# Performance work log

Measured on AMD Instinct MI355X. Metric: run time of the kernel, lower is better.

## Reference

```python
import jax, jax.numpy as jnp
import numpy as np


def ternarize_weight(w):
    # abs-mean threshold quantization to {-am, 0, +am}
    abs_mean = jnp.maximum(jnp.abs(w).mean(), 1e-5)
    thr = 0.7 * abs_mean
    q = jnp.where(w > thr, 1.0, jnp.where(w < -thr, -1.0, 0.0))
    # STE: forward value is q*abs_mean, grad flows to w as identity
    return w + jax.lax.stop_gradient(q * abs_mean - w)


def rotate_half(x):
    x1, x2 = jnp.split(x, 2, axis=-1)
    return jnp.concatenate([-x2, x1], axis=-1)


def setup_inputs() -> dict:
    key = jax.random.key(0)
    k1, k2, k3, k4, k5 = jax.random.split(key, 5)
    B, T, C, H = 2, 2048, 1024, 16
    D = C // H
    x = jax.random.normal(k1, (B, T, C), dtype=jnp.float32)
    cos = jax.random.uniform(k2, (1, 1, T, D), dtype=jnp.float32)
    sin = jax.random.uniform(k3, (1, 1, T, D), dtype=jnp.float32)
    w_qkv = jax.random.normal(k4, (3 * C, C), dtype=jnp.float32) / np.sqrt(C)
    w_proj = jax.random.normal(k5, (C, C), dtype=jnp.float32) / np.sqrt(C)
    return {"x": x, "cos": cos, "sin": sin, "w_qkv": w_qkv, "w_proj": w_proj}


def reference(x, cos, sin, w_qkv, w_proj):
    B, T, C = x.shape
    H = 16
    D = C // H
    wq = ternarize_weight(w_qkv)
    wp = ternarize_weight(w_proj)
    qkv = x @ wq.T  # [B,T,3C]
    q, k, v = jnp.split(qkv, 3, axis=-1)
    # [B,T,C] -> [B,H,T,D]
    q = q.reshape(B, T, H, D).transpose(0, 2, 1, 3)
    k = k.reshape(B, T, H, D).transpose(0, 2, 1, 3)
    v = v.reshape(B, T, H, D).transpose(0, 2, 1, 3)
    # RoPE
    q = q * cos + rotate_half(q) * sin
    k = k * cos + rotate_half(k) * sin
    # causal SDPA
    scale = 1.0 / np.sqrt(D)
    scores = jnp.einsum("bhqd,bhkd->bhqk", q, k) * scale
    causal = jnp.tril(jnp.ones((T, T), dtype=bool))
    scores = jnp.where(causal, scores, jnp.finfo(scores.dtype).min)
    attn = jax.nn.softmax(scores, axis=-1)
    y = jnp.einsum("bhqk,bhkd->bhqd", attn, v)  # [B,H,T,D]
    y = y.transpose(0, 2, 1, 3).reshape(B, T, C)
    return y @ wp.T
```

## Files before the change

kernel.cpp:

```cpp
#include <hip/hip_runtime.h>
#include <hip/hip_bf16.h>

#define B_ 2
#define T_ 2048
#define C_ 1024
#define H_ 16
#define D_ 64
#define M_ 4096
#define N3C 3072

using short8  = __attribute__((ext_vector_type(8))) short;
using floatx4 = __attribute__((ext_vector_type(4))) float;
typedef unsigned int u32;

__device__ __forceinline__ unsigned short f2b(float f) {
  __hip_bfloat16 h = __float2bfloat16(f);
  return *reinterpret_cast<unsigned short*>(&h);
}
__device__ __forceinline__ float b2f(unsigned short u) {
  union { unsigned int i; float f; } x; x.i = ((unsigned int)u) << 16; return x.f;
}
__device__ __forceinline__ u32 pk2(float a, float b) {
  float2 t; t.x = a; t.y = b;
  __hip_bfloat162 p = __float22bfloat162_rn(t);
  return *reinterpret_cast<u32*>(&p);
}

#if __has_builtin(__builtin_amdgcn_exp2f)
__device__ __forceinline__ float ex2(float x) { return __builtin_amdgcn_exp2f(x); }
#else
__device__ __forceinline__ float ex2(float x) { return exp2f(x); }
#endif

__device__ __forceinline__ void gll16(const void* g, void* l) {
  __builtin_amdgcn_global_load_lds((const __attribute__((address_space(1))) u32*)g,
                                   (__attribute__((address_space(3))) u32*)l, 16, 0, 0);
}

#define SYNCV(N) do {                                                   \
    asm volatile("s_waitcnt vmcnt(" #N ")" ::: "memory");               \
    __builtin_amdgcn_s_barrier();                                       \
    asm volatile("" ::: "memory");                                      \
  } while (0)


__global__ void abs_sum2(const float* __restrict__ wq, const float* __restrict__ wp,
                         double* __restrict__ sums) {
  __shared__ double red[4];
  const float* w = blockIdx.y ? wp : wq;
  const int n4 = blockIdx.y ? (C_ * C_ / 4) : (3 * C_ * C_ / 4);
  int stride = gridDim.x * blockDim.x;
  double s = 0.0;
  for (int i = blockIdx.x * blockDim.x + threadIdx.x; i < n4; i += stride) {
    float4 v = ((const float4*)w)[i];
    s += (double)fabsf(v.x) + (double)fabsf(v.y) + (double)fabsf(v.z) + (double)fabsf(v.w);
  }
  #pragma unroll
  for (int off = 32; off > 0; off >>= 1)
    s += __shfl_down(s, off, 64);
  if ((threadIdx.x & 63) == 0) red[threadIdx.x >> 6] = s;
  __syncthreads();
  if (threadIdx.x == 0) atomicAdd(sums + blockIdx.y, (red[0] + red[1]) + (red[2] + red[3]));
}

__global__ void tern_cvt(const float* __restrict__ wq, const float* __restrict__ wp,
                         const float* __restrict__ x,
                         unsigned short* __restrict__ oq, unsigned short* __restrict__ op,
                         unsigned short* __restrict__ xb,
                         const double* __restrict__ sums, float* __restrict__ ams) {
  const int NQ = 3 * C_ * C_;
  const int NP = C_ * C_;
  int i = blockIdx.x * blockDim.x + threadIdx.x;
  float am0 = fmaxf((float)(sums[0] * (1.0 / NQ)), 1e-5f);
  float am1 = fmaxf((float)(sums[1] * (1.0 / NP)), 1e-5f);
  if (i == 0) { ams[0] = am0; ams[1] = am1; }
  if (i < NQ) {
    float thr = 0.7f * am0, v = wq[i];
    oq[i] = (v > thr) ? 0x3F80u : ((v < -thr) ? 0xBF80u : 0u);
  } else if (i < NQ + NP) {
    int j = i - NQ;
    float thr = 0.7f * am1, v = wp[j];
    op[j] = (v > thr) ? 0x3F80u : ((v < -thr) ? 0xBF80u : 0u);
  } else {
    int j = i - NQ - NP;
    float4 v = ((const float4*)x)[j];
    ushort4 o; o.x = f2b(v.x); o.y = f2b(v.y); o.z = f2b(v.z); o.w = f2b(v.w);
    ((ushort4*)xb)[j] = o;
  }
}


__global__ __launch_bounds__(512) void gemm_qkv(const unsigned short* __restrict__ A,
                                                const unsigned short* __restrict__ W,
                                                const float* __restrict__ scale_ptr,
                                                const float* __restrict__ cosp,
                                                const float* __restrict__ sinp,
                                                unsigned short* __restrict__ Qb,
                                                unsigned short* __restrict__ Kb,
                                                unsigned short* __restrict__ Vtb) {
  const int K = C_;
  __shared__ __attribute__((aligned(16))) unsigned short As[3][256 * 32];
  __shared__ __attribute__((aligned(16))) unsigned short Ws[3][192 * 32];
  const int tid = threadIdx.x, lane = tid & 63, wv = tid >> 6;
  const int m = lane & 15, g = lane >> 4;
  const int m0 = blockIdx.y * 256, n0 = blockIdx.x * 192;
  const int wm = (wv >> 1) * 64, wn = wv & 1;
  const bool wlow = (wv < 4);

  const int srow16 = lane >> 2;
  const int skoff = (lane & 3) * 8;
  const unsigned short* ga0 = A + (size_t)(m0 + wv * 32 + srow16) * K + skoff;
  const unsigned short* ga1 = A + (size_t)(m0 + wv * 32 + 16 + srow16) * K + skoff;
  const unsigned short* gw0 = W + (size_t)(n0 + wv * 16 + srow16) * K + skoff;
  const unsigned short* gw1 = W + (size_t)(n0 + 128 + wv * 16 + srow16) * K + skoff;
  const int oA0 = (wv * 32) * 32;
  const int oA1 = (wv * 32 + 16) * 32;
  const int oW0 = (wv * 16) * 32;
  const int oW1 = (128 + wv * 16) * 32;

  floatx4 acc[4][6] = {};

#define QSTAGE(T) do {                                                    \
    gll16(ga0, &As[T][oA0]); gll16(ga1, &As[T][oA1]);                     \
    gll16(gw0, &Ws[T][oW0]);                                              \
    if (wlow) gll16(gw1, &Ws[T][oW1]);                                    \
    ga0 += 32; ga1 += 32; gw0 += 32; gw1 += 32;                           \
  } while (0)

#define QSYNC() do {                                                      \
    if (wlow) asm volatile("s_waitcnt vmcnt(4)" ::: "memory");            \
    else      asm volatile("s_waitcnt vmcnt(3)" ::: "memory");            \
    __builtin_amdgcn_s_barrier();                                         \
    asm volatile("" ::: "memory");                                        \
  } while (0)

#define QCOMP(T) do {                                                     \
    short8 af[4], wf[6];                                                  \
    _Pragma("unroll")                                                     \
    for (int r = 0; r < 4; r++)                                           \
      af[r] = *(const short8*)&As[T][(wm + r * 16 + m) * 32 + g * 8];     \
    _Pragma("unroll")                                                     \
    for (int j = 0; j < 6; j++)                                           \
      wf[j] = *(const short8*)&Ws[T][((2 * j + wn) * 16 + m) * 32 + g * 8]; \
    _Pragma("unroll")                                                     \
    for (int r = 0; r < 4; r++)                                           \
      _Pragma("unroll")                                                   \
      for (int j = 0; j < 6; j++)                                         \
        acc[r][j] = __builtin_amdgcn_mfma_f32_16x16x32_bf16(af[r], wf[j], acc[r][j], 0, 0, 0); \
  } while (0)

  QSTAGE(0);
  QSTAGE(1);
  QSYNC();
  for (int tt = 0; tt < 10; ++tt) {
    QSTAGE(2); QCOMP(0); QSYNC();
    QSTAGE(0); QCOMP(1); QSYNC();
    QSTAGE(1); QCOMP(2); QSYNC();
  }
  QCOMP(0); SYNCV(0);
  QCOMP(1);
#undef QSTAGE
#undef QSYNC
#undef QCOMP

  const float am = *scale_ptr;
  #pragma unroll
  for (int j = 0; j < 6; j++) {
    const int colb = n0 + (2 * j + wn) * 16;
    const int sect = colb >> 10;
    const int h = (colb >> 6) & 15;
    const int pb = colb & 63;
    const int p = pb + m;
    if (sect < 2) {
      unsigned short* dst = sect ? Kb : Qb;
      const float sc = sect ? am : am * 0.18033688011112042f;
      const bool hi = (pb & 32) != 0;
      #pragma unroll
      for (int r = 0; r < 4; r++)
        #pragma unroll
        for (int i = 0; i < 4; i++) {
          int row = m0 + wm + r * 16 + g * 4 + i;
          int t = row & (T_ - 1), b = row >> 11;
          float cv = cosp[t * 64 + p], sv = sinp[t * 64 + p];
          float a = acc[r][j][i], pt = acc[r][j ^ 1][i];
          float val = hi ? (a * cv + pt * sv) : (a * cv - pt * sv);
          dst[((size_t)(b * H_ + h) * T_ + t) * 64 + p] = f2b(val * sc);
        }
    } else {
      #pragma unroll
      for (int r = 0; r < 4; r++)
        #pragma unroll
        for (int i = 0; i < 4; i++) {
          int row = m0 + wm + r * 16 + g * 4 + i;
          int t = row & (T_ - 1), b = row >> 11;
          size_t hbase = (size_t)(b * H_ + h) * 64 * T_;
          Vtb[hbase + (size_t)p * T_ + t] = f2b(acc[r][j][i] * am);
        }
    }
  }
}


__global__ __launch_bounds__(256) void gemm_proj(const unsigned short* __restrict__ A,
                                                 const unsigned short* __restrict__ W,
                                                 const float* __restrict__ scale_ptr,
                                                 float* __restrict__ Cout) {
  const int K = C_, N = C_;
  __shared__ __attribute__((aligned(16))) unsigned short As[3][128 * 32];
  __shared__ __attribute__((aligned(16))) unsigned short Ws[3][128 * 32];
  const int tid = threadIdx.x, lane = tid & 63, wv = tid >> 6;
  const int m = lane & 15, g = lane >> 4;
  const int m0 = blockIdx.y * 128, n0 = blockIdx.x * 128;
  const int wm = (wv >> 1) * 64, wn = (wv & 1) * 64;

  const int srow16 = lane >> 2;
  const int skoff = (lane & 3) * 8;
  const unsigned short* ga0 = A + (size_t)(m0 + wv * 32 + srow16) * K + skoff;
  const unsigned short* ga1 = A + (size_t)(m0 + wv * 32 + 16 + srow16) * K + skoff;
  const unsigned short* gw0 = W + (size_t)(n0 + wv * 32 + srow16) * K + skoff;
  const unsigned short* gw1 = W + (size_t)(n0 + wv * 32 + 16 + srow16) * K + skoff;
  const int o0 = (wv * 32) * 32;
  const int o1 = (wv * 32 + 16) * 32;

  floatx4 acc[4][4] = {};

#define PSTAGE(T) do {                                                    \
    gll16(ga0, &As[T][o0]); gll16(ga1, &As[T][o1]);                       \
    gll16(gw0, &Ws[T][o0]); gll16(gw1, &Ws[T][o1]);                       \
    ga0 += 32; ga1 += 32; gw0 += 32; gw1 += 32;                           \
  } while (0)

#define PCOMP(T) do {                                                     \
    short8 af[4], wf[4];                                                  \
    _Pragma("unroll")                                                     \
    for (int r = 0; r < 4; r++)                                           \
      af[r] = *(const short8*)&As[T][(wm + r * 16 + m) * 32 + g * 8];     \
    _Pragma("unroll")                                                     \
    for (int c = 0; c < 4; c++)                                           \
      wf[c] = *(const short8*)&Ws[T][(wn + c * 16 + m) * 32 + g * 8];     \
    _Pragma("unroll")                                                     \
    for (int r = 0; r < 4; r++)                                           \
      _Pragma("unroll")                                                   \
      for (int c = 0; c < 4; c++)                                         \
        acc[r][c] = __builtin_amdgcn_mfma_f32_16x16x32_bf16(af[r], wf[c], acc[r][c], 0, 0, 0); \
  } while (0)

  PSTAGE(0);
  PSTAGE(1);
  SYNCV(4);
  for (int tt = 0; tt < 10; ++tt) {
    PSTAGE(2); PCOMP(0); SYNCV(4);
    PSTAGE(0); PCOMP(1); SYNCV(4);
    PSTAGE(1); PCOMP(2); SYNCV(4);
  }
  PCOMP(0); SYNCV(0);
  PCOMP(1);
#undef PSTAGE
#undef PCOMP

  const float scale = *scale_ptr;
  #pragma unroll
  for (int r = 0; r < 4; r++)
    #pragma unroll
    for (int c = 0; c < 4; c++)
      #pragma unroll
      for (int i = 0; i < 4; i++) {
        int row = m0 + wm + r * 16 + g * 4 + i;
        int col = n0 + wn + c * 16 + m;
        Cout[(size_t)row * N + col] = acc[r][c][i] * scale;
      }
}


__global__ __launch_bounds__(256) void flash_mfma(const unsigned short* __restrict__ Qb,
                                                  const unsigned short* __restrict__ Kb,
                                                  const unsigned short* __restrict__ Vtb,
                                                  unsigned short* __restrict__ Y) {
  __shared__ __align__(16) unsigned short Ktile[2][64][64];
  __shared__ __align__(16) unsigned short Vtile[2][64][64];
  __shared__ __align__(16) unsigned short Plds[4][16][72];
  const int lane = threadIdx.x & 63;
  const int wv = threadIdx.x >> 6;
  const int m = lane & 15, g = lane >> 4;
  const int gid = blockIdx.x;
  const int xcd = gid & 7, j = gid >> 3;
  const int bh = xcd * 4 + (j & 3);
  const int s = 31 - (j >> 2);
  const int b = bh >> 4, h = bh & 15;
  const size_t hb = (size_t)bh * T_ * 64;
  const unsigned short* Kbh = Kb + hb;
  const unsigned short* Vbh = Vtb + hb;
  const int r8 = lane >> 3, cc8 = lane & 7;
  const int gcol = ((cc8 ^ r8) << 3);

  const int ntiles = s + 1;
  const int qbase = s * 64 + wv * 16;
  const int q_glob = qbase + m;

  const unsigned short* qp = Qb + hb + (size_t)(qbase + m) * 64 + g * 8;
  short8 qf0 = *(const short8*)qp;
  short8 qf1 = *(const short8*)(qp + 32);

  short8 ones;
  #pragma unroll
  for (int i = 0; i < 8; i++) ones[i] = (short)0x3F80;

  floatx4 O[4] = {};
  floatx4 accl = {};

  #pragma unroll
  for (int cc = 0; cc < 2; cc++) {
    int row = wv * 16 + cc * 8;
    gll16(Kbh + (size_t)(row + r8) * 64 + gcol, &Ktile[0][row][0]);
    gll16(Vbh + (size_t)(row + r8) * T_ + gcol, &Vtile[0][row][0]);
  }

  for (int kt = 0; kt < ntiles; kt++) {
    const int buf = kt & 1;
    const int kb = kt * 64;
    __syncthreads();
    if (kt + 1 < ntiles) {
      const int kb2 = kb + 64;
      #pragma unroll
      for (int cc = 0; cc < 2; cc++) {
        int row = wv * 16 + cc * 8;
        gll16(Kbh + (size_t)(kb2 + row + r8) * 64 + gcol, &Ktile[1 - buf][row][0]);
        gll16(Vbh + (size_t)(row + r8) * T_ + kb2 + gcol, &Vtile[1 - buf][row][0]);
      }
    }
    floatx4 S[4];
    __builtin_amdgcn_s_setprio(1);
    #pragma unroll
    for (int mt = 0; mt < 4; mt++) {
      int row = mt * 16 + m;
      short8 kf0 = *(const short8*)&Ktile[buf][row][(g ^ (m & 7)) << 3];
      short8 kf1 = *(const short8*)&Ktile[buf][row][((g + 4) ^ (m & 7)) << 3];
      floatx4 sv = {};
      sv = __builtin_amdgcn_mfma_f32_16x16x32_bf16(kf0, qf0, sv, 0, 0, 0);
      sv = __builtin_amdgcn_mfma_f32_16x16x32_bf16(kf1, qf1, sv, 0, 0, 0);
      S[mt] = sv;
    }
    __builtin_amdgcn_s_setprio(0);
    if (kt + 1 < ntiles) {
      #pragma unroll
      for (int mt = 0; mt < 4; mt++) {
        uint2 w;
        w.x = pk2(ex2(S[mt][0]), ex2(S[mt][1]));
        w.y = pk2(ex2(S[mt][2]), ex2(S[mt][3]));
        *(uint2*)&Plds[wv][m][mt * 16 + g * 4] = w;
      }
    } else {
      #pragma unroll
      for (int mt = 0; mt < 4; mt++) {
        float e[4];
        #pragma unroll
        for (int r = 0; r < 4; r++) {
          int kg = kb + mt * 16 + g * 4 + r;
          e[r] = (kg <= q_glob) ? ex2(S[mt][r]) : 0.f;
        }
        uint2 w;
        w.x = pk2(e[0], e[1]);
        w.y = pk2(e[2], e[3]);
        *(uint2*)&Plds[wv][m][mt * 16 + g * 4] = w;
      }
    }
    short8 pa0 = *(const short8*)&Plds[wv][m][g * 8];
    short8 pa1 = *(const short8*)&Plds[wv][m][32 + g * 8];
    __builtin_amdgcn_s_setprio(1);
    #pragma unroll
    for (int nt = 0; nt < 4; nt++) {
      int row = nt * 16 + m;
      short8 v0 = *(const short8*)&Vtile[buf][row][(g ^ (m & 7)) << 3];
      short8 v1 = *(const short8*)&Vtile[buf][row][((g + 4) ^ (m & 7)) << 3];
      O[nt] = __builtin_amdgcn_mfma_f32_16x16x32_bf16(pa0, v0, O[nt], 0, 0, 0);
      O[nt] = __builtin_amdgcn_mfma_f32_16x16x32_bf16(pa1, v1, O[nt], 0, 0, 0);
    }
    accl = __builtin_amdgcn_mfma_f32_16x16x32_bf16(pa0, ones, accl, 0, 0, 0);
    accl = __builtin_amdgcn_mfma_f32_16x16x32_bf16(pa1, ones, accl, 0, 0, 0);
    __builtin_amdgcn_s_setprio(0);
  }

  float li[4];
  #pragma unroll
  for (int r = 0; r < 4; r++) li[r] = 1.0f / accl[r];
  #pragma unroll
  for (int nt = 0; nt < 4; nt++)
    #pragma unroll
    for (int r = 0; r < 4; r++) {
      int trow = qbase + g * 4 + r;
      int col = h * 64 + nt * 16 + m;
      Y[(size_t)(b * T_ + trow) * C_ + col] = f2b(O[nt][r] * li[r]);
    }
}


extern "C" void kernel_launch(void* const* d_in, const int* in_sizes, int n_in,
                              void* d_out, int out_size, void* d_ws, size_t ws_size,
                              hipStream_t stream) {
  (void)in_sizes; (void)n_in; (void)out_size; (void)ws_size;
  const float* x      = (const float*)d_in[0];
  const float* cosp   = (const float*)d_in[1];
  const float* sinp   = (const float*)d_in[2];
  const float* w_qkv  = (const float*)d_in[3];
  const float* w_proj = (const float*)d_in[4];
  float* out = (float*)d_out;

  char* ws = (char*)d_ws;
  double* sums = (double*)ws;
  float*  ams  = (float*)(ws + 16);
  unsigned short* wqkv_b  = (unsigned short*)(ws + 256);
  unsigned short* wproj_b = wqkv_b + (size_t)N3C * C_;
  unsigned short* xb      = wproj_b + (size_t)C_ * C_;
  unsigned short* Qb      = xb + (size_t)M_ * C_;
  unsigned short* Kb      = Qb + (size_t)B_ * H_ * T_ * D_;
  unsigned short* Vtb     = Kb + (size_t)B_ * H_ * T_ * D_;
  unsigned short* yb      = Vtb + (size_t)B_ * H_ * T_ * D_;

  hipMemsetAsync(sums, 0, 16, stream);
  abs_sum2<<<dim3(256, 2), 256, 0, stream>>>(w_qkv, w_proj, sums);
  tern_cvt<<<(4 * C_ * C_ + M_ * C_ / 4) / 256, 256, 0, stream>>>(w_qkv, w_proj, x,
                                                                  wqkv_b, wproj_b, xb,
                                                                  sums, ams);
  gemm_qkv<<<dim3(N3C / 192, M_ / 256), 512, 0, stream>>>(xb, wqkv_b, ams + 0,
                                                          cosp, sinp, Qb, Kb, Vtb);
  flash_mfma<<<1024, 256, 0, stream>>>(Qb, Kb, Vtb, yb);
  gemm_proj<<<dim3(C_ / 128, M_ / 128), 256, 0, stream>>>(yb, wproj_b, ams + 1, out);
}
```

Before: 201.8 us.

## Store ternary weights as 8-bit codes and expand to bf16 in registers

The ternary weight matrices are now written as one byte per element, with codes whose bits become a bf16 ±2 when shifted into the high byte. Both GEMMs load these bytes into LDS, expand them to bf16 fragments with shifts and masks, and fold the extra factor of two into the output scale. This halves weight write and read traffic plus LDS footprint, at the cost of extra ALU work for each fragment. The QKV GEMM also shrinks from 512 threads with 256-row tiles to 256 threads with 128-row tiles, doubling the block count.

Result: faster. 196.2 us (median of 2 runs) (-2.8%).

```diff
diff --git a/kernel.cpp b/kernel.cpp
--- a/kernel.cpp
+++ b/kernel.cpp
@@ -17,9 +17,6 @@
   __hip_bfloat16 h = __float2bfloat16(f);
   return *reinterpret_cast<unsigned short*>(&h);
 }
-__device__ __forceinline__ float b2f(unsigned short u) {
-  union { unsigned int i; float f; } x; x.i = ((unsigned int)u) << 16; return x.f;
-}
 __device__ __forceinline__ u32 pk2(float a, float b) {
   float2 t; t.x = a; t.y = b;
   __hip_bfloat162 p = __float22bfloat162_rn(t);
@@ -42,6 +39,17 @@
     __builtin_amdgcn_s_barrier();                                       \
     asm volatile("" ::: "memory");                                      \
   } while (0)
+
+__device__ __forceinline__ short8 xpnd(uint2 p) {
+  u32 a = p.x, b = p.y;
+  u32 d0 = ((a << 8) & 0x0000FF00u) | ((a << 16) & 0xFF000000u);
+  u32 d1 = ((a >> 8) & 0x0000FF00u) | (a & 0xFF000000u);
+  u32 d2 = ((b << 8) & 0x0000FF00u) | ((b << 16) & 0xFF000000u);
+  u32 d3 = ((b >> 8) & 0x0000FF00u) | (b & 0xFF000000u);
+  union { u32 d[4]; short8 s; } r;
+  r.d[0] = d0; r.d[1] = d1; r.d[2] = d2; r.d[3] = d3;
+  return r.s;
+}
 
 
 __global__ void abs_sum2(const float* __restrict__ wq, const float* __restrict__ wp,
@@ -65,7 +73,7 @@
 
 __global__ void tern_cvt(const float* __restrict__ wq, const float* __restrict__ wp,
                          const float* __restrict__ x,
-                         unsigned short* __restrict__ oq, unsigned short* __restrict__ op,
+                         unsigned char* __restrict__ oq, unsigned char* __restrict__ op,
                          unsigned short* __restrict__ xb,
                          const double* __restrict__ sums, float* __restrict__ ams) {
   const int NQ = 3 * C_ * C_;
@@ -76,11 +84,11 @@
   if (i == 0) { ams[0] = am0; ams[1] = am1; }
   if (i < NQ) {
     float thr = 0.7f * am0, v = wq[i];
-    oq[i] = (v > thr) ? 0x3F80u : ((v < -thr) ? 0xBF80u : 0u);
+    oq[i] = (v > thr) ? 0x40u : ((v < -thr) ? 0xC0u : 0u);
   } else if (i < NQ + NP) {
     int j = i - NQ;
     float thr = 0.7f * am1, v = wp[j];
-    op[j] = (v > thr) ? 0x3F80u : ((v < -thr) ? 0xBF80u : 0u);
+    op[j] = (v > thr) ? 0x40u : ((v < -thr) ? 0xC0u : 0u);
   } else {
     int j = i - NQ - NP;
     float4 v = ((const float4*)x)[j];
@@ -90,8 +98,8 @@
 }
 
 
-__global__ __launch_bounds__(512) void gemm_qkv(const unsigned short* __restrict__ A,
-                                                const unsigned short* __restrict__ W,
+__global__ __launch_bounds__(256) void gemm_qkv(const unsigned short* __restrict__ A,
+                                                const unsigned char* __restrict__ W8,
                                                 const float* __restrict__ scale_ptr,
                                                 const float* __restrict__ cosp,
                                                 const float* __restrict__ sinp,
@@ -99,24 +107,24 @@
                                                 unsigned short* __restrict__ Kb,
                                                 unsigned short* __restrict__ Vtb) {
   const int K = C_;
-  __shared__ __attribute__((aligned(16))) unsigned short As[3][256 * 32];
-  __shared__ __attribute__((aligned(16))) unsigned short Ws[3][192 * 32];
+  __shared__ __attribute__((aligned(16))) unsigned short As[3][128 * 32];
+  __shared__ __attribute__((aligned(16))) unsigned char  Ws[3][192 * 32];
   const int tid = threadIdx.x, lane = tid & 63, wv = tid >> 6;
   const int m = lane & 15, g = lane >> 4;
-  const int m0 = blockIdx.y * 256, n0 = blockIdx.x * 192;
+  const int m0 = blockIdx.y * 128, n0 = blockIdx.x * 192;
   const int wm = (wv >> 1) * 64, wn = wv & 1;
-  const bool wlow = (wv < 4);
+  const bool wlow = (wv < 2);
 
   const int srow16 = lane >> 2;
   const int skoff = (lane & 3) * 8;
   const unsigned short* ga0 = A + (size_t)(m0 + wv * 32 + srow16) * K + skoff;
   const unsigned short* ga1 = A + (size_t)(m0 + wv * 32 + 16 + srow16) * K + skoff;
-  const unsigned short* gw0 = W + (size_t)(n0 + wv * 16 + srow16) * K + skoff;
-  const unsigned short* gw1 = W + (size_t)(n0 + 128 + wv * 16 + srow16) * K + skoff;
+  const unsigned char* gw0 = W8 + (size_t)(n0 + wv * 32 + (lane >> 1)) * K + (lane & 1) * 16;
+  const unsigned char* gw1 = W8 + (size_t)(n0 + 128 + wv * 32 + (lane >> 1)) * K + (lane & 1) * 16;
   const int oA0 = (wv * 32) * 32;
   const int oA1 = (wv * 32 + 16) * 32;
-  const int oW0 = (wv * 16) * 32;
-  const int oW1 = (128 + wv * 16) * 32;
+  const int oW0 = (wv * 32) * 32;
+  const int oW1 = ((128 + wv * 32)) * 32;
 
   floatx4 acc[4][6] = {};
 
@@ -141,7 +149,7 @@
       af[r] = *(const short8*)&As[T][(wm + r * 16 + m) * 32 + g * 8];     \
     _Pragma("unroll")                                                     \
     for (int j = 0; j < 6; j++)                                           \
-      wf[j] = *(const short8*)&Ws[T][((2 * j + wn) * 16 + m) * 32 + g * 8]; \
+      wf[j] = xpnd(*(const uint2*)&Ws[T][((2 * j + wn) * 16 + m) * 32 + g * 8]); \
     _Pragma("unroll")                                                     \
     for (int r = 0; r < 4; r++)                                           \
       _Pragma("unroll")                                                   \
@@ -164,6 +172,7 @@
 #undef QCOMP
 
   const float am = *scale_ptr;
+  const float amh = am * 0.5f;
   #pragma unroll
   for (int j = 0; j < 6; j++) {
     const int colb = n0 + (2 * j + wn) * 16;
@@ -173,7 +182,7 @@
     const int p = pb + m;
     if (sect < 2) {
       unsigned short* dst = sect ? Kb : Qb;
-      const float sc = sect ? am : am * 0.18033688011112042f;
+      const float sc = sect ? amh : amh * 0.18033688011112042f;
       const bool hi = (pb & 32) != 0;
       #pragma unroll
       for (int r = 0; r < 4; r++)
@@ -194,7 +203,7 @@
           int row = m0 + wm + r * 16 + g * 4 + i;
           int t = row & (T_ - 1), b = row >> 11;
           size_t hbase = (size_t)(b * H_ + h) * 64 * T_;
-          Vtb[hbase + (size_t)p * T_ + t] = f2b(acc[r][j][i] * am);
+          Vtb[hbase + (size_t)p * T_ + t] = f2b(acc[r][j][i] * amh);
         }
     }
   }
@@ -202,12 +211,12 @@
 
 
 __global__ __launch_bounds__(256) void gemm_proj(const unsigned short* __restrict__ A,
-                                                 const unsigned short* __restrict__ W,
+                                                 const unsigned char* __restrict__ W8,
                                                  const float* __restrict__ scale_ptr,
                                                  float* __restrict__ Cout) {
   const int K = C_, N = C_;
   __shared__ __attribute__((aligned(16))) unsigned short As[3][128 * 32];
-  __shared__ __attribute__((aligned(16))) unsigned short Ws[3][128 * 32];
+  __shared__ __attribute__((aligned(16))) unsigned char  Ws[3][128 * 32];
   const int tid = threadIdx.x, lane = tid & 63, wv = tid >> 6;
   const int m = lane & 15, g = lane >> 4;
   const int m0 = blockIdx.y * 128, n0 = blockIdx.x * 128;
@@ -217,17 +226,17 @@
   const int skoff = (lane & 3) * 8;
   const unsigned short* ga0 = A + (size_t)(m0 + wv * 32 + srow16) * K + skoff;
   const unsigned short* ga1 = A + (size_t)(m0 + wv * 32 + 16 + srow16) * K + skoff;
-  const unsigned short* gw0 = W + (size_t)(n0 + wv * 32 + srow16) * K + skoff;
-  const unsigned short* gw1 = W + (size_t)(n0 + wv * 32 + 16 + srow16) * K + skoff;
-  const int o0 = (wv * 32) * 32;
-  const int o1 = (wv * 32 + 16) * 32;
+  const unsigned char* gw0 = W8 + (size_t)(n0 + wv * 32 + (lane >> 1)) * K + (lane & 1) * 16;
+  const int oA0 = (wv * 32) * 32;
+  const int oA1 = (wv * 32 + 16) * 32;
+  const int oW0 = (wv * 32) * 32;
 
   floatx4 acc[4][4] = {};
 
 #define PSTAGE(T) do {                                                    \
-    gll16(ga0, &As[T][o0]); gll16(ga1, &As[T][o1]);                       \
-    gll16(gw0, &Ws[T][o0]); gll16(gw1, &Ws[T][o1]);                       \
-    ga0 += 32; ga1 += 32; gw0 += 32; gw1 += 32;                           \
+    gll16(ga0, &As[T][oA0]); gll16(ga1, &As[T][oA1]);                     \
+    gll16(gw0, &Ws[T][oW0]);                                              \
+    ga0 += 32; ga1 += 32; gw0 += 32;                                      \
   } while (0)
 
 #define PCOMP(T) do {                                                     \
@@ -237,7 +246,7 @@
       af[r] = *(const short8*)&As[T][(wm + r * 16 + m) * 32 + g * 8];     \
     _Pragma("unroll")                                                     \
     for (int c = 0; c < 4; c++)                                           \
-      wf[c] = *(const short8*)&Ws[T][(wn + c * 16 + m) * 32 + g * 8];     \
+      wf[c] = xpnd(*(const uint2*)&Ws[T][(wn + c * 16 + m) * 32 + g * 8]); \
     _Pragma("unroll")                                                     \
     for (int r = 0; r < 4; r++)                                           \
       _Pragma("unroll")                                                   \
@@ -247,18 +256,18 @@
 
   PSTAGE(0);
   PSTAGE(1);
-  SYNCV(4);
+  SYNCV(3);
   for (int tt = 0; tt < 10; ++tt) {
-    PSTAGE(2); PCOMP(0); SYNCV(4);
-    PSTAGE(0); PCOMP(1); SYNCV(4);
-    PSTAGE(1); PCOMP(2); SYNCV(4);
+    PSTAGE(2); PCOMP(0); SYNCV(3);
+    PSTAGE(0); PCOMP(1); SYNCV(3);
+    PSTAGE(1); PCOMP(2); SYNCV(3);
   }
   PCOMP(0); SYNCV(0);
   PCOMP(1);
 #undef PSTAGE
 #undef PCOMP
 
-  const float scale = *scale_ptr;
+  const float scale = *scale_ptr * 0.5f;
   #pragma unroll
   for (int r = 0; r < 4; r++)
     #pragma unroll
@@ -408,21 +417,21 @@
   char* ws = (char*)d_ws;
   double* sums = (double*)ws;
   float*  ams  = (float*)(ws + 16);
-  unsigned short* wqkv_b  = (unsigned short*)(ws + 256);
-  unsigned short* wproj_b = wqkv_b + (size_t)N3C * C_;
-  unsigned short* xb      = wproj_b + (size_t)C_ * C_;
-  unsigned short* Qb      = xb + (size_t)M_ * C_;
-  unsigned short* Kb      = Qb + (size_t)B_ * H_ * T_ * D_;
-  unsigned short* Vtb     = Kb + (size_t)B_ * H_ * T_ * D_;
-  unsigned short* yb      = Vtb + (size_t)B_ * H_ * T_ * D_;
+  unsigned char*  wqkv_b8  = (unsigned char*)(ws + 256);
+  unsigned char*  wproj_b8 = wqkv_b8 + (size_t)N3C * C_;
+  unsigned short* xb  = (unsigned short*)(wproj_b8 + (size_t)C_ * C_);
+  unsigned short* Qb  = xb + (size_t)M_ * C_;
+  unsigned short* Kb  = Qb + (size_t)B_ * H_ * T_ * D_;
+  unsigned short* Vtb = Kb + (size_t)B_ * H_ * T_ * D_;
+  unsigned short* yb  = Vtb + (size_t)B_ * H_ * T_ * D_;
 
   hipMemsetAsync(sums, 0, 16, stream);
   abs_sum2<<<dim3(256, 2), 256, 0, stream>>>(w_qkv, w_proj, sums);
   tern_cvt<<<(4 * C_ * C_ + M_ * C_ / 4) / 256, 256, 0, stream>>>(w_qkv, w_proj, x,
-                                                                  wqkv_b, wproj_b, xb,
+                                                                  wqkv_b8, wproj_b8, xb,
                                                                   sums, ams);
-  gemm_qkv<<<dim3(N3C / 192, M_ / 256), 512, 0, stream>>>(xb, wqkv_b, ams + 0,
+  gemm_qkv<<<dim3(N3C / 192, M_ / 128), 256, 0, stream>>>(xb, wqkv_b8, ams + 0,
                                                           cosp, sinp, Qb, Kb, Vtb);
   flash_mfma<<<1024, 256, 0, stream>>>(Qb, Kb, Vtb, yb);
-  gemm_proj<<<dim3(C_ / 128, M_ / 128), 256, 0, stream>>>(yb, wproj_b, ams + 1, out);
-}
+  gemm_proj<<<dim3(C_ / 128, M_ / 128), 256, 0, stream>>>(yb, wproj_b8, ams + 1, out);
+}
```
